# Optimization experiments

Measured on AMD Instinct MI355X. Metric: run time of the kernel, lower is better.

Reference implementation:

```python
import jax, jax.numpy as jnp
import numpy as np


def setup_inputs() -> dict:
    key = jax.random.key(0)
    k1, k2, k3, k4 = jax.random.split(key, 4)
    Q = jax.random.normal(k1, (32, 32, 128), dtype=jnp.float32)
    D = jax.random.normal(k2, (512, 180, 128), dtype=jnp.float32)
    q_mask = jax.random.randint(k3, (32, 32), 0, 2, dtype=jnp.int32)
    d_mask = jax.random.randint(k4, (512, 180), 0, 2, dtype=jnp.int32)
    return {"Q": Q, "D": D, "q_mask": q_mask, "d_mask": d_mask}


def reference(Q, D, q_mask, d_mask):
    # ColBERT MaxSim late-interaction scoring (ColBERT_List_qa.score)
    # Q: [q, m, h], D: [d, n, h]; masks zero out padding token embeddings.
    Qm = Q * q_mask.astype(Q.dtype)[..., None]              # [q, m, h]
    Dm = D * d_mask.astype(D.dtype)[..., None]              # [d, n, h]
    sim = jnp.einsum("qmh,dnh->qdmn", Qm, Dm)               # [q, d, m, n]
    scores = sim.max(axis=-1).sum(axis=-1)                  # max over doc tokens n, sum over query tokens m -> [q, d]
    return scores
```

## Files before the change

kernel.cpp:

```cpp
#include <hip/hip_runtime.h>
#include <hip/hip_bf16.h>

typedef __attribute__((ext_vector_type(8))) short short8;
typedef __attribute__((ext_vector_type(4))) float f32x4;

#define NQ 32
#define NM 32
#define NH 128
#define ND 512
#define NN 180
#define NTMAX 12
#define MTILES 64
#define LSTR 136

#define QFRAG_BYTES (MTILES * 4 * 64 * 16)
#define QSTART_OFF  QFRAG_BYTES
#define T2_OFF      (QSTART_OFF + 33 * 4)

static __device__ __forceinline__ unsigned short f2bf(float x) {
  __hip_bfloat16 h = __float2bfloat16(x);
  return __builtin_bit_cast(unsigned short, h);
}

static __device__ __forceinline__ uint4 pack8(float4 a, float4 b) {
  unsigned int x = (unsigned)f2bf(a.x) | ((unsigned)f2bf(a.y) << 16);
  unsigned int y = (unsigned)f2bf(a.z) | ((unsigned)f2bf(a.w) << 16);
  unsigned int z = (unsigned)f2bf(b.x) | ((unsigned)f2bf(b.y) << 16);
  unsigned int u = (unsigned)f2bf(b.z) | ((unsigned)f2bf(b.w) << 16);
  return make_uint4(x, y, z, u);
}

__global__ __launch_bounds__(256) void prep_q_compact(
    const float* __restrict__ Q, const int* __restrict__ qmask,
    unsigned short* __restrict__ Qb, int* __restrict__ qstart_g,
    int* __restrict__ t2_g) {
  __shared__ unsigned short src_tok[NQ * NM];
  __shared__ int rtot[16];
  const int tid = threadIdx.x;
  const int lane = tid & 63;
  const int wv = tid >> 6;

  int flags[4], pres[4];
  #pragma unroll
  for (int r = 0; r < 4; ++r) {
    int idx = r * 256 + tid;
    int f = qmask[idx];
    unsigned long long bal = __ballot(f != 0);
    int pre = __popcll(bal & ((1ull << lane) - 1ull));
    if (lane == 63) rtot[r * 4 + wv] = pre + (f ? 1 : 0);
    flags[r] = f;
    pres[r] = pre;
  }
  __syncthreads();
  int total = 0;
  int chunkbase[4];
  {
    int run = 0;
    #pragma unroll
    for (int r = 0; r < 4; ++r) {
      chunkbase[r] = run + ((wv >= 1) ? rtot[r * 4 + 0] : 0) +
                           ((wv >= 2) ? rtot[r * 4 + 1] : 0) +
                           ((wv >= 3) ? rtot[r * 4 + 2] : 0);
      run += rtot[r * 4 + 0] + rtot[r * 4 + 1] + rtot[r * 4 + 2] + rtot[r * 4 + 3];
    }
    total = run;
  }
  #pragma unroll
  for (int r = 0; r < 4; ++r) {
    int idx = r * 256 + tid;
    int pos = chunkbase[r] + pres[r];
    if (flags[r]) src_tok[pos] = (unsigned short)idx;
    if (blockIdx.x == 0 && (idx & 31) == 0) qstart_g[idx >> 5] = pos;
  }
  __syncthreads();
  if (blockIdx.x == 0 && tid == 0) {
    qstart_g[32] = total;
    int T = (total + 15) >> 4;
    t2_g[0] = (T + 1) >> 1;
  }

  {
    int s = blockIdx.x * 256 + tid;
    int t2 = s >> 8, ks = (s >> 6) & 3, ln = s & 63;
    int col = t2 * 16 + (ln & 15);
    int kk = ks * 32 + (ln >> 4) * 8;
    uint4 o = make_uint4(0u, 0u, 0u, 0u);
    if (col < total) {
      int tok = src_tok[col];
      const float* src = Q + tok * NH + kk;
      float4 a = *reinterpret_cast<const float4*>(src);
      float4 b = *reinterpret_cast<const float4*>(src + 4);
      o = pack8(a, b);
    }
    reinterpret_cast<uint4*>(Qb)[s] = o;
  }
}

__global__ __launch_bounds__(512, 4) void fused_maxsim(
    const float* __restrict__ D, const int* __restrict__ dmask,
    const unsigned short* __restrict__ Qb, const int* __restrict__ qstart_g,
    const int* __restrict__ t2_g, float* __restrict__ out) {
  __shared__ unsigned short Dlds[192 * LSTR];
  __shared__ float colmax[MTILES * 16];
  __shared__ unsigned short mapinv[192];
  __shared__ int wtot[4];
  const int d = blockIdx.x;
  const int tid = threadIdx.x;
  const int lane = tid & 63;
  const int w = tid >> 6;
  const float NEG = -__builtin_inff();

  int flag = 0, pre = 0;
  if (tid < NN) flag = dmask[d * NN + tid];
  if (tid < 192) {
    unsigned long long bal = __ballot(flag != 0);
    pre = __popcll(bal & ((1ull << lane) - 1ull));
    if (lane == 63) wtot[w] = pre + (flag ? 1 : 0);
  }
  __syncthreads();
  const int cnt = wtot[0] + wtot[1] + wtot[2];
  if (tid < 192 && flag) {
    int base = (w >= 1 ? wtot[0] : 0) + (w >= 2 ? wtot[1] : 0);
    mapinv[pre + base] = (unsigned short)tid;
  }
  __syncthreads();

  const int T2 = t2_g[0];

  short8 Qp0[4], Qp1[4];
  {
    const int t0 = w * 2;
    #pragma unroll
    for (int ks = 0; ks < 4; ++ks) {
      Qp0[ks] = *reinterpret_cast<const short8*>(
          reinterpret_cast<const char*>(Qb) +
          (((t0 * 4 + ks) << 10) + (lane << 4)));
      Qp1[ks] = *reinterpret_cast<const short8*>(
          reinterpret_cast<const char*>(Qb) +
          ((((t0 + 1) * 4 + ks) << 10) + (lane << 4)));
    }
  }

  const int ntc = (cnt + 15) >> 4;
  {
    const int rg = tid >> 5;
    const int c4 = tid & 31;
    const int nrows = ntc * 16;
    #pragma unroll 4
    for (int base = 0; base < nrows; base += 16) {
      int dr = base + rg;
      uint2 o = make_uint2(0u, 0u);
      if (dr < cnt) {
        int sr = mapinv[dr];
        float4 v = reinterpret_cast<const float4*>(D)[(size_t)(d * NN + sr) * 32 + c4];
        o.x = (unsigned)f2bf(v.x) | ((unsigned)f2bf(v.y) << 16);
        o.y = (unsigned)f2bf(v.z) | ((unsigned)f2bf(v.w) << 16);
      }
      *reinterpret_cast<uint2*>(&Dlds[dr * LSTR + c4 * 4]) = o;
    }
  }
  __syncthreads();

  const int bl = lane & 15;
  const int bg = lane >> 4;

  #pragma unroll 1
  for (int tp = w; tp < T2; tp += 8) {
    const int t0 = tp * 2;

    short8 Qf0[4], Qf1[4];
    if (tp == w) {
      #pragma unroll
      for (int ks = 0; ks < 4; ++ks) { Qf0[ks] = Qp0[ks]; Qf1[ks] = Qp1[ks]; }
    } else {
      #pragma unroll
      for (int ks = 0; ks < 4; ++ks) {
        Qf0[ks] = *reinterpret_cast<const short8*>(
            reinterpret_cast<const char*>(Qb) +
            (((t0 * 4 + ks) << 10) + (lane << 4)));
        Qf1[ks] = *reinterpret_cast<const short8*>(
            reinterpret_cast<const char*>(Qb) +
            ((((t0 + 1) * 4 + ks) << 10) + (lane << 4)));
      }
    }

    float run0 = NEG, run1 = NEG;

    #pragma unroll 2
    for (int nt = 0; nt < ntc; ++nt) {
      short8 Da[4];
      #pragma unroll
      for (int ks = 0; ks < 4; ++ks)
        Da[ks] = *reinterpret_cast<const short8*>(
            &Dlds[(nt * 16 + bl) * LSTR + ks * 32 + bg * 8]);

      f32x4 acc0 = {0.f, 0.f, 0.f, 0.f};
      f32x4 acc1 = acc0;
      #pragma unroll
      for (int ks = 0; ks < 4; ++ks) {
        acc0 = __builtin_amdgcn_mfma_f32_16x16x32_bf16(Da[ks], Qf0[ks], acc0, 0, 0, 0);
        acc1 = __builtin_amdgcn_mfma_f32_16x16x32_bf16(Da[ks], Qf1[ks], acc1, 0, 0, 0);
      }

      if (nt * 16 + 16 > cnt) {
        const int rlim = cnt - nt * 16 - bg * 4;
        float v0 = NEG, v1 = NEG;
        #pragma unroll
        for (int j = 0; j < 4; ++j) {
          v0 = fmaxf(v0, (j < rlim) ? acc0[j] : NEG);
          v1 = fmaxf(v1, (j < rlim) ? acc1[j] : NEG);
        }
        run0 = fmaxf(run0, v0);
        run1 = fmaxf(run1, v1);
      } else {
        run0 = fmaxf(run0, fmaxf(fmaxf(acc0[0], acc0[1]), fmaxf(acc0[2], acc0[3])));
        run1 = fmaxf(run1, fmaxf(fmaxf(acc1[0], acc1[1]), fmaxf(acc1[2], acc1[3])));
      }
    }

    if (cnt < NN) {
      run0 = fmaxf(run0, 0.f);
      run1 = fmaxf(run1, 0.f);
    }

    run0 = fmaxf(run0, __shfl_xor(run0, 16));
    run0 = fmaxf(run0, __shfl_xor(run0, 32));
    run1 = fmaxf(run1, __shfl_xor(run1, 16));
    run1 = fmaxf(run1, __shfl_xor(run1, 32));

    if (lane < 16) {
      colmax[t0 * 16 + lane] = run0;
      colmax[(t0 + 1) * 16 + lane] = run1;
    }
  }
  __syncthreads();

  if (tid < NQ) {
    const int s0 = qstart_g[tid];
    const int s1 = qstart_g[tid + 1];
    float s = 0.f;
    for (int i = s0; i < s1; ++i) s += colmax[i];
    out[tid * ND + d] = s;
  }
}

extern "C" void kernel_launch(void* const* d_in, const int* in_sizes, int n_in,
                              void* d_out, int out_size, void* d_ws, size_t ws_size,
                              hipStream_t stream) {
  const float* Q = (const float*)d_in[0];
  const float* D = (const float*)d_in[1];
  const int* qmask = (const int*)d_in[2];
  const int* dmask = (const int*)d_in[3];
  float* out = (float*)d_out;

  unsigned short* Qb = (unsigned short*)d_ws;
  int* qstart_g = (int*)((char*)d_ws + QSTART_OFF);
  int* t2_g = (int*)((char*)d_ws + T2_OFF);

  prep_q_compact<<<64, 256, 0, stream>>>(Q, qmask, Qb, qstart_g, t2_g);
  fused_maxsim<<<ND, 512, 0, stream>>>(D, dmask, Qb, qstart_g, t2_g, out);
}
```

Baseline: 21.68 us.

## Process two documents per block, prefetching the second into registers during compute

Each block now handles two documents, launching half as many blocks. The second document's rows are loaded from global memory into registers and converted to bf16 before the first document's MFMA loop, then written to LDS afterwards, so their global load latency is hidden behind compute. The cost is double LDS use, a larger register footprint (occupancy hint lowered from 4 to 2), Q fragments reloaded on every iteration, and only 256 blocks to spread across the CUs.

```diff
diff --git a/kernel.cpp b/kernel.cpp
--- a/kernel.cpp
+++ b/kernel.cpp
@@ -9,7 +9,6 @@
 #define NH 128
 #define ND 512
 #define NN 180
-#define NTMAX 12
 #define MTILES 64
 #define LSTR 136
 
@@ -78,7 +77,6 @@
     int T = (total + 15) >> 4;
     t2_g[0] = (T + 1) >> 1;
   }
-
   {
     int s = blockIdx.x * 256 + tid;
     int t2 = s >> 8, ks = (s >> 6) & 3, ln = s & 63;
@@ -96,104 +94,104 @@
   }
 }
 
-__global__ __launch_bounds__(512, 4) void fused_maxsim(
+__global__ __launch_bounds__(512, 2) void fused_maxsim2(
     const float* __restrict__ D, const int* __restrict__ dmask,
     const unsigned short* __restrict__ Qb, const int* __restrict__ qstart_g,
     const int* __restrict__ t2_g, float* __restrict__ out) {
-  __shared__ unsigned short Dlds[192 * LSTR];
-  __shared__ float colmax[MTILES * 16];
-  __shared__ unsigned short mapinv[192];
-  __shared__ int wtot[4];
-  const int d = blockIdx.x;
+  __shared__ unsigned short Dlds0[192 * LSTR];
+  __shared__ unsigned short Dlds1[192 * LSTR];
+  __shared__ float colmax[2][MTILES * 16];
+  __shared__ unsigned short mapinv0[192], mapinv1[192];
+  __shared__ int wtot[8];
+  const int b = blockIdx.x;
+  const int d0 = b;
+  const int d1 = b + 256;
   const int tid = threadIdx.x;
   const int lane = tid & 63;
   const int w = tid >> 6;
   const float NEG = -__builtin_inff();
 
   int flag = 0, pre = 0;
-  if (tid < NN) flag = dmask[d * NN + tid];
-  if (tid < 192) {
+  const int sub = tid & 255;
+  const int grp = tid >> 8;
+  const int dsel = grp ? d1 : d0;
+  if (sub < NN) flag = dmask[dsel * NN + sub];
+  if (sub < 192) {
     unsigned long long bal = __ballot(flag != 0);
     pre = __popcll(bal & ((1ull << lane) - 1ull));
     if (lane == 63) wtot[w] = pre + (flag ? 1 : 0);
   }
   __syncthreads();
-  const int cnt = wtot[0] + wtot[1] + wtot[2];
-  if (tid < 192 && flag) {
-    int base = (w >= 1 ? wtot[0] : 0) + (w >= 2 ? wtot[1] : 0);
-    mapinv[pre + base] = (unsigned short)tid;
-  }
-  __syncthreads();
-
+  const int cnt0 = wtot[0] + wtot[1] + wtot[2];
+  const int cnt1 = wtot[4] + wtot[5] + wtot[6];
+  if (sub < 192 && flag) {
+    int wb = grp * 4;
+    int base = ((w - wb) >= 1 ? wtot[wb] : 0) + ((w - wb) >= 2 ? wtot[wb + 1] : 0);
+    if (grp == 0) mapinv0[pre + base] = (unsigned short)sub;
+    else          mapinv1[pre + base] = (unsigned short)sub;
+  }
+  __syncthreads();
+
+  const int ntc0 = (cnt0 + 15) >> 4;
+  const int ntc1 = (cnt1 + 15) >> 4;
   const int T2 = t2_g[0];
-
-  short8 Qp0[4], Qp1[4];
+  const int rg = tid >> 5;
+  const int c4 = tid & 31;
+  const int bl = lane & 15;
+  const int bg = lane >> 4;
+
   {
-    const int t0 = w * 2;
-    #pragma unroll
-    for (int ks = 0; ks < 4; ++ks) {
-      Qp0[ks] = *reinterpret_cast<const short8*>(
-          reinterpret_cast<const char*>(Qb) +
-          (((t0 * 4 + ks) << 10) + (lane << 4)));
-      Qp1[ks] = *reinterpret_cast<const short8*>(
-          reinterpret_cast<const char*>(Qb) +
-          ((((t0 + 1) * 4 + ks) << 10) + (lane << 4)));
-    }
-  }
-
-  const int ntc = (cnt + 15) >> 4;
-  {
-    const int rg = tid >> 5;
-    const int c4 = tid & 31;
-    const int nrows = ntc * 16;
+    const int nrows = ntc0 * 16;
     #pragma unroll 4
     for (int base = 0; base < nrows; base += 16) {
       int dr = base + rg;
       uint2 o = make_uint2(0u, 0u);
-      if (dr < cnt) {
-        int sr = mapinv[dr];
-        float4 v = reinterpret_cast<const float4*>(D)[(size_t)(d * NN + sr) * 32 + c4];
+      if (dr < cnt0) {
+        int sr = mapinv0[dr];
+        float4 v = reinterpret_cast<const float4*>(D)[(size_t)(d0 * NN + sr) * 32 + c4];
         o.x = (unsigned)f2bf(v.x) | ((unsigned)f2bf(v.y) << 16);
         o.y = (unsigned)f2bf(v.z) | ((unsigned)f2bf(v.w) << 16);
       }
-      *reinterpret_cast<uint2*>(&Dlds[dr * LSTR + c4 * 4]) = o;
-    }
-  }
-  __syncthreads();
-
-  const int bl = lane & 15;
-  const int bg = lane >> 4;
+      *reinterpret_cast<uint2*>(&Dlds0[dr * LSTR + c4 * 4]) = o;
+    }
+  }
+  __syncthreads();
+
+  const int nrows1 = ntc1 * 16;
+  uint2 st1[12];
+  #pragma unroll
+  for (int i = 0; i < 12; ++i) {
+    int base = i * 16;
+    int dr = base + rg;
+    uint2 o = make_uint2(0u, 0u);
+    if (base < nrows1 && dr < cnt1) {
+      int sr = mapinv1[dr];
+      float4 v = reinterpret_cast<const float4*>(D)[(size_t)(d1 * NN + sr) * 32 + c4];
+      o.x = (unsigned)f2bf(v.x) | ((unsigned)f2bf(v.y) << 16);
+      o.y = (unsigned)f2bf(v.z) | ((unsigned)f2bf(v.w) << 16);
+    }
+    st1[i] = o;
+  }
 
   #pragma unroll 1
   for (int tp = w; tp < T2; tp += 8) {
     const int t0 = tp * 2;
-
     short8 Qf0[4], Qf1[4];
-    if (tp == w) {
-      #pragma unroll
-      for (int ks = 0; ks < 4; ++ks) { Qf0[ks] = Qp0[ks]; Qf1[ks] = Qp1[ks]; }
-    } else {
-      #pragma unroll
-      for (int ks = 0; ks < 4; ++ks) {
-        Qf0[ks] = *reinterpret_cast<const short8*>(
-            reinterpret_cast<const char*>(Qb) +
-            (((t0 * 4 + ks) << 10) + (lane << 4)));
-        Qf1[ks] = *reinterpret_cast<const short8*>(
-            reinterpret_cast<const char*>(Qb) +
-            ((((t0 + 1) * 4 + ks) << 10) + (lane << 4)));
-      }
-    }
-
+    #pragma unroll
+    for (int ks = 0; ks < 4; ++ks) {
+      Qf0[ks] = *reinterpret_cast<const short8*>(
+          reinterpret_cast<const char*>(Qb) + (((t0 * 4 + ks) << 10) + (lane << 4)));
+      Qf1[ks] = *reinterpret_cast<const short8*>(
+          reinterpret_cast<const char*>(Qb) + ((((t0 + 1) * 4 + ks) << 10) + (lane << 4)));
+    }
     float run0 = NEG, run1 = NEG;
-
     #pragma unroll 2
-    for (int nt = 0; nt < ntc; ++nt) {
+    for (int nt = 0; nt < ntc0; ++nt) {
       short8 Da[4];
       #pragma unroll
       for (int ks = 0; ks < 4; ++ks)
         Da[ks] = *reinterpret_cast<const short8*>(
-            &Dlds[(nt * 16 + bl) * LSTR + ks * 32 + bg * 8]);
-
+            &Dlds0[(nt * 16 + bl) * LSTR + ks * 32 + bg * 8]);
       f32x4 acc0 = {0.f, 0.f, 0.f, 0.f};
       f32x4 acc1 = acc0;
       #pragma unroll
@@ -201,9 +199,8 @@
         acc0 = __builtin_amdgcn_mfma_f32_16x16x32_bf16(Da[ks], Qf0[ks], acc0, 0, 0, 0);
         acc1 = __builtin_amdgcn_mfma_f32_16x16x32_bf16(Da[ks], Qf1[ks], acc1, 0, 0, 0);
       }
-
-      if (nt * 16 + 16 > cnt) {
-        const int rlim = cnt - nt * 16 - bg * 4;
+      if (nt * 16 + 16 > cnt0) {
+        const int rlim = cnt0 - nt * 16 - bg * 4;
         float v0 = NEG, v1 = NEG;
         #pragma unroll
         for (int j = 0; j < 4; ++j) {
@@ -217,30 +214,88 @@
         run1 = fmaxf(run1, fmaxf(fmaxf(acc1[0], acc1[1]), fmaxf(acc1[2], acc1[3])));
       }
     }
-
-    if (cnt < NN) {
-      run0 = fmaxf(run0, 0.f);
-      run1 = fmaxf(run1, 0.f);
-    }
-
+    if (cnt0 < NN) { run0 = fmaxf(run0, 0.f); run1 = fmaxf(run1, 0.f); }
     run0 = fmaxf(run0, __shfl_xor(run0, 16));
     run0 = fmaxf(run0, __shfl_xor(run0, 32));
     run1 = fmaxf(run1, __shfl_xor(run1, 16));
     run1 = fmaxf(run1, __shfl_xor(run1, 32));
-
     if (lane < 16) {
-      colmax[t0 * 16 + lane] = run0;
-      colmax[(t0 + 1) * 16 + lane] = run1;
-    }
-  }
-  __syncthreads();
-
-  if (tid < NQ) {
-    const int s0 = qstart_g[tid];
-    const int s1 = qstart_g[tid + 1];
+      colmax[0][t0 * 16 + lane] = run0;
+      colmax[0][(t0 + 1) * 16 + lane] = run1;
+    }
+  }
+
+  #pragma unroll
+  for (int i = 0; i < 12; ++i) {
+    int base = i * 16;
+    if (base < nrows1) {
+      int dr = base + rg;
+      *reinterpret_cast<uint2*>(&Dlds1[dr * LSTR + c4 * 4]) = st1[i];
+    }
+  }
+  __syncthreads();
+
+  #pragma unroll 1
+  for (int tp = w; tp < T2; tp += 8) {
+    const int t0 = tp * 2;
+    short8 Qf0[4], Qf1[4];
+    #pragma unroll
+    for (int ks = 0; ks < 4; ++ks) {
+      Qf0[ks] = *reinterpret_cast<const short8*>(
+          reinterpret_cast<const char*>(Qb) + (((t0 * 4 + ks) << 10) + (lane << 4)));
+      Qf1[ks] = *reinterpret_cast<const short8*>(
+          reinterpret_cast<const char*>(Qb) + ((((t0 + 1) * 4 + ks) << 10) + (lane << 4)));
+    }
+    float run0 = NEG, run1 = NEG;
+    #pragma unroll 2
+    for (int nt = 0; nt < ntc1; ++nt) {
+      short8 Da[4];
+      #pragma unroll
+      for (int ks = 0; ks < 4; ++ks)
+        Da[ks] = *reinterpret_cast<const short8*>(
+            &Dlds1[(nt * 16 + bl) * LSTR + ks * 32 + bg * 8]);
+      f32x4 acc0 = {0.f, 0.f, 0.f, 0.f};
+      f32x4 acc1 = acc0;
+      #pragma unroll
+      for (int ks = 0; ks < 4; ++ks) {
+        acc0 = __builtin_amdgcn_mfma_f32_16x16x32_bf16(Da[ks], Qf0[ks], acc0, 0, 0, 0);
+        acc1 = __builtin_amdgcn_mfma_f32_16x16x32_bf16(Da[ks], Qf1[ks], acc1, 0, 0, 0);
+      }
+      if (nt * 16 + 16 > cnt1) {
+        const int rlim = cnt1 - nt * 16 - bg * 4;
+        float v0 = NEG, v1 = NEG;
+        #pragma unroll
+        for (int j = 0; j < 4; ++j) {
+          v0 = fmaxf(v0, (j < rlim) ? acc0[j] : NEG);
+          v1 = fmaxf(v1, (j < rlim) ? acc1[j] : NEG);
+        }
+        run0 = fmaxf(run0, v0);
+        run1 = fmaxf(run1, v1);
+      } else {
+        run0 = fmaxf(run0, fmaxf(fmaxf(acc0[0], acc0[1]), fmaxf(acc0[2], acc0[3])));
+        run1 = fmaxf(run1, fmaxf(fmaxf(acc1[0], acc1[1]), fmaxf(acc1[2], acc1[3])));
+      }
+    }
+    if (cnt1 < NN) { run0 = fmaxf(run0, 0.f); run1 = fmaxf(run1, 0.f); }
+    run0 = fmaxf(run0, __shfl_xor(run0, 16));
+    run0 = fmaxf(run0, __shfl_xor(run0, 32));
+    run1 = fmaxf(run1, __shfl_xor(run1, 16));
+    run1 = fmaxf(run1, __shfl_xor(run1, 32));
+    if (lane < 16) {
+      colmax[1][t0 * 16 + lane] = run0;
+      colmax[1][(t0 + 1) * 16 + lane] = run1;
+    }
+  }
+  __syncthreads();
+
+  if (tid < 64) {
+    const int q = tid & 31;
+    const int dd = tid >> 5;
+    const int s0 = qstart_g[q];
+    const int s1 = qstart_g[q + 1];
     float s = 0.f;
-    for (int i = s0; i < s1; ++i) s += colmax[i];
-    out[tid * ND + d] = s;
+    for (int i = s0; i < s1; ++i) s += colmax[dd][i];
+    out[q * ND + (dd ? d1 : d0)] = s;
   }
 }
 
@@ -258,5 +313,5 @@
   int* t2_g = (int*)((char*)d_ws + T2_OFF);
 
   prep_q_compact<<<64, 256, 0, stream>>>(Q, qmask, Qb, qstart_g, t2_g);
-  fused_maxsim<<<ND, 512, 0, stream>>>(D, dmask, Qb, qstart_g, t2_g, out);
-}
+  fused_maxsim2<<<ND / 2, 512, 0, stream>>>(D, dmask, Qb, qstart_g, t2_g, out);
+}
```

Result: slower. 24.53 us (+13.2%).
